# Kernel tuning notes

Hardware: AMD Instinct MI355X
Metric: run time of the kernel (lower is better)

## Reference

```python
import jax, jax.numpy as jnp
import numpy as np

# ---- MERU-style Lorentz geometry helpers (space components, implicit time) ----

def _time(x, curv):
    # x: [..., D] space component; time = sqrt(1/curv + ||x||^2)
    return jnp.sqrt(1.0 / curv + jnp.sum(x * x, axis=-1))


def pairwise_dist(x, y, curv, eps=1e-8):
    # Lorentzian inner product for all pairs: <x,y>_L = x.y - x_t*y_t  -> [N, M]
    xt = _time(x, curv)
    yt = _time(y, curv)
    inner = jnp.einsum('nd,md->nm', x, y) - xt[:, None] * yt[None, :]
    c_xyl = -curv * inner  # >= 1 on the hyperboloid
    return jnp.arccosh(jnp.clip(c_xyl, 1.0 + eps, None)) / jnp.sqrt(curv)


def oxy_angle(x, y, curv, eps=1e-8):
    # exterior angle at x of geodesic triangle (origin, x, y); elementwise over batch
    xt = _time(x, curv)
    yt = _time(y, curv)
    c_xyl = curv * (jnp.sum(x * y, axis=-1) - xt * yt)  # <= -1
    acos_numer = yt + c_xyl * xt
    acos_denom = jnp.linalg.norm(x, axis=-1) * jnp.sqrt(jnp.clip(c_xyl * c_xyl - 1.0, 0.0, None))
    acos_input = acos_numer / (acos_denom + eps)
    return jnp.arccos(jnp.clip(acos_input, -1.0 + eps, 1.0 - eps))


def half_aperture(x, curv, min_radius=0.1, eps=1e-6):
    asin_input = 2.0 * min_radius / (jnp.linalg.norm(x, axis=-1) * jnp.sqrt(curv) + eps)
    return jnp.arcsin(jnp.clip(asin_input, -1.0 + eps, 1.0 - eps))


def soft_cross_entropy(logits, target_probs):
    # torch.nn.CrossEntropyLoss with probability targets (rows need not sum to 1)
    return jnp.mean(-jnp.sum(target_probs * jax.nn.log_softmax(logits, axis=-1), axis=-1))


def entailment_loss(fa, fb, curv, eps=1e-6):
    ang = oxy_angle(fa, fb, curv)
    ap = half_aperture(fa, curv, eps=eps)
    return jnp.mean(jnp.clip(ang - ap, 0.0, None))


def setup_inputs() -> dict:
    key = jax.random.key(0)
    k1, k2, k3, k4 = jax.random.split(key, 4)
    B, D = 4096, 512
    return {
        'image_features': jax.random.normal(k1, (B, D), dtype=jnp.float32),
        'dna_features': jax.random.normal(k2, (B, D), dtype=jnp.float32),
        'text_features': jax.random.normal(k3, (B, D), dtype=jnp.float32),
        'labels': jax.random.randint(k4, (B,), 0, 500, dtype=jnp.int64),
        'logit_scale': jnp.float32(10.0),
        'curv': jnp.float32(1.0),
    }


ENTAIL_WEIGHT = 0.2


def reference(image_features, dna_features, text_features, labels, logit_scale, curv):
    # world_size == 1: gathered features == local features
    label_mat = (labels[None, :] == labels[:, None]).astype(jnp.float32)  # [B, B]

    feats = [image_features, dna_features, text_features]  # idx 0=image, 1=dna, 2=text

    contrastive_losses = []
    entail_losses = []
    for ia in range(3):
        for ib in range(3):
            if ia == ib:
                continue
            sim_ab = -pairwise_dist(feats[ia], feats[ib], curv)
            sim_ba = -pairwise_dist(feats[ib], feats[ia], curv)
            contrastive_losses.append(soft_cross_entropy(logit_scale * sim_ab, label_mat))
            contrastive_losses.append(soft_cross_entropy(logit_scale * sim_ba, label_mat))
            # 2D features branch: entailment only for (dna, image) ordering
            if ia == 1 and ib == 0:
                entail_losses.append(entailment_loss(feats[1], feats[0], curv, eps=1e-6))
            elif ia == 0 and ib == 1:
                entail_losses.append(entailment_loss(feats[1], feats[0], curv, eps=1e-6))

    contrastive_total = sum(contrastive_losses) / len(contrastive_losses)
    entail_total = sum(entail_losses) / len(entail_losses)
    total = contrastive_total + ENTAIL_WEIGHT * entail_total
    return total, contrastive_total, entail_total
```

## Files before the change

### kernel.cpp

```cpp
#include <hip/hip_runtime.h>
#include <stdint.h>

#define B_SZ 4096
#define D_SZ 512
#define SHIFT 64.0f

typedef __attribute__((ext_vector_type(4))) float floatx4;
typedef __attribute__((ext_vector_type(2))) long lng2;
typedef unsigned char u8;
typedef unsigned int u32;

#define GLD_LDS16(gp, sp)                                                              \
    __builtin_amdgcn_global_load_lds(                                                  \
        (const __attribute__((address_space(1))) void*)(gp),                           \
        (__attribute__((address_space(3))) void*)(sp), 16, 0, 0)

#define FP8MFMA(accv, av, bv)                                                          \
    accv = __builtin_amdgcn_mfma_f32_16x16x32_fp8_fp8(av, bv, accv, 0, 0, 0)

__global__ __launch_bounds__(256) void prep_kernel(
    const float* __restrict__ img, const float* __restrict__ dna,
    const float* __restrict__ txt, const float* __restrict__ curv_p,
    const int* __restrict__ labels, int* __restrict__ hist,
    u8* __restrict__ f8, float* __restrict__ times,
    float* __restrict__ zero_f, float* __restrict__ ent_partial) {
    __shared__ int lhist[512];
    __shared__ float red[4];
    int t = threadIdx.x;
    int gid = blockIdx.x * 256 + t;
    if (gid < 49155) zero_f[gid] = 0.0f;

    if (blockIdx.x == 0) {
        lhist[t] = 0; lhist[t + 256] = 0;
        __syncthreads();
        for (int n = t; n < B_SZ; n += 256) atomicAdd(&lhist[labels[n]], 1);
        __syncthreads();
        hist[t] = lhist[t]; hist[t + 256] = lhist[t + 256];
    }

    int wave = gid >> 6;
    int lane = t & 63;
    const float* src = (wave < B_SZ) ? img : (wave < 2 * B_SZ) ? dna : txt;
    int row = wave & (B_SZ - 1);
    const float* p = src + row * D_SZ + lane * 8;
    float4 v0 = *(const float4*)(p);
    float4 v1 = *(const float4*)(p + 4);
    float ss = v0.x*v0.x + v0.y*v0.y + v0.z*v0.z + v0.w*v0.w
             + v1.x*v1.x + v1.y*v1.y + v1.z*v1.z + v1.w*v1.w;
    u32 w0 = __builtin_amdgcn_cvt_pk_fp8_f32(v0.x, v0.y, 0, false);
    w0 = __builtin_amdgcn_cvt_pk_fp8_f32(v0.z, v0.w, w0, true);
    u32 w1 = __builtin_amdgcn_cvt_pk_fp8_f32(v1.x, v1.y, 0, false);
    w1 = __builtin_amdgcn_cvt_pk_fp8_f32(v1.z, v1.w, w1, true);
    uint2 pk; pk.x = w0; pk.y = w1;
    int gperm = (lane & 56) | ((lane & 3) << 1) | ((lane >> 2) & 1);
    *(uint2*)(f8 + (size_t)wave * D_SZ + gperm * 8) = pk;

    bool isdna = (wave >= B_SZ) && (wave < 2 * B_SZ);
    float dot = 0.0f, ssy = 0.0f;
    if (isdna) {
        const float* y = img + row * D_SZ + lane * 8;
        float4 y0 = *(const float4*)y, y1 = *(const float4*)(y + 4);
        dot = v0.x*y0.x + v0.y*y0.y + v0.z*y0.z + v0.w*y0.w
            + v1.x*y1.x + v1.y*y1.y + v1.z*y1.z + v1.w*y1.w;
        ssy = y0.x*y0.x + y0.y*y0.y + y0.z*y0.z + y0.w*y0.w
            + y1.x*y1.x + y1.y*y1.y + y1.z*y1.z + y1.w*y1.w;
    }
    #pragma unroll
    for (int m = 1; m < 64; m <<= 1) {
        ss += __shfl_xor(ss, m);
        if (isdna) { dot += __shfl_xor(dot, m); ssy += __shfl_xor(ssy, m); }
    }
    float curv = curv_p[0];
    float ep = 0.0f;
    if (lane == 0) {
        float xt = sqrtf(1.0f / curv + ss);
        times[wave] = xt;
        if (isdna) {
            float yt = sqrtf(1.0f / curv + ssy);
            float nx = sqrtf(ss);
            float c = curv * (dot - xt * yt);
            float numer = yt + c * xt;
            float denom = nx * sqrtf(fmaxf(c * c - 1.0f, 0.0f));
            float ai = numer / (denom + 1e-8f);
            ai = fminf(fmaxf(ai, -1.0f + 1e-8f), 1.0f - 1e-8f);
            float ang = acosf(ai);
            float as_in = 0.2f / (nx * sqrtf(curv) + 1e-6f);
            as_in = fminf(fmaxf(as_in, -1.0f + 1e-6f), 1.0f - 1e-6f);
            float ap = asinf(as_in);
            ep = fmaxf(ang - ap, 0.0f);
        }
    }
    if (blockIdx.x >= 1024 && blockIdx.x < 2048) {
        if (lane == 0) red[t >> 6] = ep;
        __syncthreads();
        if (t == 0) ent_partial[blockIdx.x - 1024] = red[0] + red[1] + red[2] + red[3];
    }
}

__global__ __launch_bounds__(512, 4) void gemm_epi_kernel(
    const u8* __restrict__ f8, const float* __restrict__ times,
    const int* __restrict__ labels,
    const float* __restrict__ ls_p, const float* __restrict__ curv_p,
    float* __restrict__ rsum_e, float* __restrict__ rsum_t,
    float* __restrict__ csum_e, float* __restrict__ csum_t) {
    __shared__ u8 sA[4][128 * 64];
    __shared__ u8 sB[4][128 * 64];

    int z = blockIdx.z;
    int pa = (z == 2) ? 1 : 0;
    int pb = (z == 0) ? 1 : 2;
    const u8* A  = f8 + (size_t)pa * (B_SZ * D_SZ);
    const u8* Bm = f8 + (size_t)pb * (B_SZ * D_SZ);

    int t = threadIdx.x;
    int rowBlk = blockIdx.y * 128;
    int colBlk = blockIdx.x * 128;
    int wave = t >> 6, lane = t & 63;
    int wr = wave >> 1;
    int wc = wave & 1;

    int chunk = (t & 3) ^ ((t >> 3) & 3);
    const u8* gA = A  + (size_t)(rowBlk + (t >> 2)) * D_SZ + chunk * 16;
    const u8* gB = Bm + (size_t)(colBlk + (t >> 2)) * D_SZ + chunk * 16;

    int q = lane >> 4, s = lane & 15;
    int slot16 = (q ^ ((s >> 1) & 3)) << 4;
    int aBase = (wr * 32 + s) * 64 + slot16;
    int bBase = (wc * 64 + s) * 64 + slot16;

    floatx4 acc[2][4];
    #pragma unroll
    for (int ii = 0; ii < 2; ++ii)
        #pragma unroll
        for (int j = 0; j < 4; ++j) acc[ii][j] = (floatx4){0.f, 0.f, 0.f, 0.f};

    {
        GLD_LDS16(gA,       &sA[0][wave * 1024]);
        GLD_LDS16(gB,       &sB[0][wave * 1024]);
        GLD_LDS16(gA + 64,  &sA[1][wave * 1024]);
        GLD_LDS16(gB + 64,  &sB[1][wave * 1024]);
        GLD_LDS16(gA + 128, &sA[2][wave * 1024]);
        GLD_LDS16(gB + 128, &sB[2][wave * 1024]);
    }

    #pragma unroll
    for (int si = 0; si < D_SZ / 64; ++si) {
        const int cur = si & 3;
        asm volatile("s_waitcnt lgkmcnt(0)" ::: "memory");
        if (si < 6)      { asm volatile("s_waitcnt vmcnt(4)" ::: "memory"); }
        else if (si == 6){ asm volatile("s_waitcnt vmcnt(2)" ::: "memory"); }
        else             { asm volatile("s_waitcnt vmcnt(0)" ::: "memory"); }
        asm volatile("s_barrier" ::: "memory");
        if (si < 5) {
            const int nxb = (si + 3) & 3;
            const int ko  = (si + 3) * 64;
            GLD_LDS16(gA + ko, &sA[nxb][wave * 1024]);
            GLD_LDS16(gB + ko, &sB[nxb][wave * 1024]);
        }
        const u8* pA = &sA[cur][0];
        const u8* pB = &sB[cur][0];
        lng2 a0 = *(const lng2*)(pA + aBase);
        lng2 a1 = *(const lng2*)(pA + aBase + 1024);
        lng2 b0 = *(const lng2*)(pB + bBase);
        lng2 b1 = *(const lng2*)(pB + bBase + 1024);
        lng2 b2 = *(const lng2*)(pB + bBase + 2048);
        lng2 b3 = *(const lng2*)(pB + bBase + 3072);
        __builtin_amdgcn_s_setprio(1);
        FP8MFMA(acc[0][0], a0.x, b0.x); FP8MFMA(acc[0][1], a0.x, b1.x);
        FP8MFMA(acc[0][2], a0.x, b2.x); FP8MFMA(acc[0][3], a0.x, b3.x);
        FP8MFMA(acc[1][0], a1.x, b0.x); FP8MFMA(acc[1][1], a1.x, b1.x);
        FP8MFMA(acc[1][2], a1.x, b2.x); FP8MFMA(acc[1][3], a1.x, b3.x);
        FP8MFMA(acc[0][0], a0.y, b0.y); FP8MFMA(acc[0][1], a0.y, b1.y);
        FP8MFMA(acc[0][2], a0.y, b2.y); FP8MFMA(acc[0][3], a0.y, b3.y);
        FP8MFMA(acc[1][0], a1.y, b0.y); FP8MFMA(acc[1][1], a1.y, b1.y);
        FP8MFMA(acc[1][2], a1.y, b2.y); FP8MFMA(acc[1][3], a1.y, b3.y);
        __builtin_amdgcn_s_setprio(0);
    }

    float ls = ls_p[0];
    float curv = curv_p[0];
    float rsc = rsqrtf(curv);
    float c2 = -ls * rsc;
    float c1 = c2 * 0.69314718f;
    float sh2p = SHIFT * 1.44269504f + c2;
    const float* tA = times + pa * B_SZ;
    const float* tB = times + pb * B_SZ;

    int rowbase = rowBlk + wr * 32;
    int colbase = colBlk + wc * 64;

    float tb[4]; int lb[4]; int mcol[4];
    #pragma unroll
    for (int j = 0; j < 4; ++j) {
        mcol[j] = colbase + j * 16 + s;
        tb[j] = tB[mcol[j]];
        lb[j] = labels[mcol[j]];
    }
    float colE[4] = {0.f, 0.f, 0.f, 0.f}, colT[4] = {0.f, 0.f, 0.f, 0.f};

    float* rsE = rsum_e + z * B_SZ;
    float* rsT = rsum_t + z * B_SZ;
    float* csE = csum_e + z * B_SZ;
    float* csT = csum_t + z * B_SZ;

    #pragma unroll
    for (int ii = 0; ii < 2; ++ii) {
        int nb = rowbase + ii * 16 + q * 4;
        float cta[4]; int la[4];
        #pragma unroll
        for (int r = 0; r < 4; ++r) { cta[r] = curv * tA[nb + r]; la[r] = labels[nb + r]; }
        float re[4] = {0.f, 0.f, 0.f, 0.f}, rt[4] = {0.f, 0.f, 0.f, 0.f};
        #pragma unroll
        for (int j = 0; j < 4; ++j) {
            floatx4 a = acc[ii][j];
            #pragma unroll
            for (int r = 0; r < 4; ++r) {
                float zc = fmaf(-curv, a[r], cta[r] * tb[j]);
                zc = fmaxf(zc, 1.0f + 1e-8f);
                float lz = __log2f(zc);
                float e = __builtin_amdgcn_exp2f(fmaf(c2, lz, sh2p));
                float tl = (la[r] == lb[j]) ? fmaf(c1, lz, c1) : 0.0f;
                re[r] += e; rt[r] += tl;
                colE[j] += e; colT[j] += tl;
            }
        }
        #pragma unroll
        for (int r = 0; r < 4; ++r) {
            #pragma unroll
            for (int m = 1; m <= 8; m <<= 1) {
                re[r] += __shfl_xor(re[r], m);
                rt[r] += __shfl_xor(rt[r], m);
            }
        }
        #pragma unroll
        for (int r = 0; r < 4; ++r) {
            if (s == r) {
                atomicAdd(&rsE[nb + r], re[r]);
                atomicAdd(&rsT[nb + r], rt[r]);
            }
        }
    }
    #pragma unroll
    for (int j = 0; j < 4; ++j) {
        colE[j] += __shfl_xor(colE[j], 16); colE[j] += __shfl_xor(colE[j], 32);
        colT[j] += __shfl_xor(colT[j], 16); colT[j] += __shfl_xor(colT[j], 32);
        if (q == 0) {
            atomicAdd(&csE[mcol[j]], colE[j]);
            atomicAdd(&csT[mcol[j]], colT[j]);
        }
    }
}

__global__ __launch_bounds__(256) void finalize_kernel(
    const float* __restrict__ rsum_e, const float* __restrict__ rsum_t,
    const float* __restrict__ csum_e, const float* __restrict__ csum_t,
    const int* __restrict__ labels, const int* __restrict__ hist,
    const float* __restrict__ ent_partial,
    float* __restrict__ ce_acc, float* __restrict__ ent_acc,
    int* __restrict__ done, float* __restrict__ out) {
    __shared__ float red[4], red2[4];
    int b = blockIdx.x, tid = threadIdx.x;
    int n = b * 256 + tid;
    float Sn = (float)hist[labels[n]];
    float part = 0.0f;
    #pragma unroll
    for (int p = 0; p < 3; ++p) {
        part += Sn * (__logf(rsum_e[p * B_SZ + n]) - SHIFT) - rsum_t[p * B_SZ + n];
        part += Sn * (__logf(csum_e[p * B_SZ + n]) - SHIFT) - csum_t[p * B_SZ + n];
    }
    float ep = (b < 4) ? ent_partial[b * 256 + tid] : 0.0f;
    #pragma unroll
    for (int m = 1; m < 64; m <<= 1) {
        part += __shfl_xor(part, m);
        ep   += __shfl_xor(ep, m);
    }
    if ((tid & 63) == 0) { red[tid >> 6] = part; red2[tid >> 6] = ep; }
    __syncthreads();
    if (tid == 0) {
        atomicAdd(ce_acc, red[0] + red[1] + red[2] + red[3]);
        atomicAdd(ent_acc, red2[0] + red2[1] + red2[2] + red2[3]);
        __threadfence();
        if (atomicAdd(done, 1) == 15) {
            float ce = atomicAdd(ce_acc, 0.0f);
            float ent = atomicAdd(ent_acc, 0.0f);
            float contr = ce / (6.0f * (float)B_SZ);
            ent /= (float)B_SZ;
            out[0] = contr + 0.2f * ent;
            out[1] = contr;
            out[2] = ent;
        }
    }
}

extern "C" void kernel_launch(void* const* d_in, const int* in_sizes, int n_in,
                              void* d_out, int out_size, void* d_ws, size_t ws_size,
                              hipStream_t stream) {
    const float* img    = (const float*)d_in[0];
    const float* dna    = (const float*)d_in[1];
    const float* txt    = (const float*)d_in[2];
    const int*   labels = (const int*)d_in[3];
    const float* ls     = (const float*)d_in[4];
    const float* curv   = (const float*)d_in[5];

    char* ws = (char*)d_ws;
    u8*    f8     = (u8*)ws;
    float* times  = (float*)(ws + 6291456);
    float* rsum_e = (float*)(ws + 6340608);
    float* rsum_t = (float*)(ws + 6389760);
    float* csum_e = (float*)(ws + 6438912);
    float* csum_t = (float*)(ws + 6488064);
    float* ce_acc = (float*)(ws + 6537216);
    float* ent_acc= (float*)(ws + 6537220);
    int*   done   = (int*)  (ws + 6537224);
    float* ent_p  = (float*)(ws + 6537228);
    int*   hist   = (int*)  (ws + 6541324);

    prep_kernel<<<3072, 256, 0, stream>>>(img, dna, txt, curv, labels, hist,
                                          f8, times, rsum_e, ent_p);
    dim3 g(32, 32, 3);
    gemm_epi_kernel<<<g, 512, 0, stream>>>(f8, times, labels, ls, curv,
                                           rsum_e, rsum_t, csum_e, csum_t);
    finalize_kernel<<<16, 256, 0, stream>>>(rsum_e, rsum_t, csum_e, csum_t,
                                            labels, hist, ent_p,
                                            ce_acc, ent_acc, done, (float*)d_out);
}
```

Before: 166.8 us.

## Make GEMM kernel persistent over six tiles with cross-tile prefetch and register double-buffering

The GEMM-epilogue kernel becomes persistent. 512 blocks each walk six consecutive 128x128 tiles instead of launching one block per tile over a 3072-block grid. The first k-slices of the next tile are prefetched into shared memory during the last k-steps of the current tile, and LDS fragments are double-buffered in registers so reads for step k+1 overlap the MFMAs of step k. The goal is to hide the pipeline fill and drain and the per-block launch overhead behind useful work. In exchange, the grid is fixed at 512 blocks, the kernel uses more registers, and the tail balance across CUs may change.

```diff
diff --git a/kernel.cpp b/kernel.cpp
--- a/kernel.cpp
+++ b/kernel.cpp
@@ -106,76 +106,15 @@
     __shared__ u8 sA[4][128 * 64];
     __shared__ u8 sB[4][128 * 64];
 
-    int z = blockIdx.z;
-    int pa = (z == 2) ? 1 : 0;
-    int pb = (z == 0) ? 1 : 2;
-    const u8* A  = f8 + (size_t)pa * (B_SZ * D_SZ);
-    const u8* Bm = f8 + (size_t)pb * (B_SZ * D_SZ);
-
     int t = threadIdx.x;
-    int rowBlk = blockIdx.y * 128;
-    int colBlk = blockIdx.x * 128;
     int wave = t >> 6, lane = t & 63;
     int wr = wave >> 1;
     int wc = wave & 1;
-
     int chunk = (t & 3) ^ ((t >> 3) & 3);
-    const u8* gA = A  + (size_t)(rowBlk + (t >> 2)) * D_SZ + chunk * 16;
-    const u8* gB = Bm + (size_t)(colBlk + (t >> 2)) * D_SZ + chunk * 16;
-
     int q = lane >> 4, s = lane & 15;
     int slot16 = (q ^ ((s >> 1) & 3)) << 4;
     int aBase = (wr * 32 + s) * 64 + slot16;
     int bBase = (wc * 64 + s) * 64 + slot16;
-
-    floatx4 acc[2][4];
-    #pragma unroll
-    for (int ii = 0; ii < 2; ++ii)
-        #pragma unroll
-        for (int j = 0; j < 4; ++j) acc[ii][j] = (floatx4){0.f, 0.f, 0.f, 0.f};
-
-    {
-        GLD_LDS16(gA,       &sA[0][wave * 1024]);
-        GLD_LDS16(gB,       &sB[0][wave * 1024]);
-        GLD_LDS16(gA + 64,  &sA[1][wave * 1024]);
-        GLD_LDS16(gB + 64,  &sB[1][wave * 1024]);
-        GLD_LDS16(gA + 128, &sA[2][wave * 1024]);
-        GLD_LDS16(gB + 128, &sB[2][wave * 1024]);
-    }
-
-    #pragma unroll
-    for (int si = 0; si < D_SZ / 64; ++si) {
-        const int cur = si & 3;
-        asm volatile("s_waitcnt lgkmcnt(0)" ::: "memory");
-        if (si < 6)      { asm volatile("s_waitcnt vmcnt(4)" ::: "memory"); }
-        else if (si == 6){ asm volatile("s_waitcnt vmcnt(2)" ::: "memory"); }
-        else             { asm volatile("s_waitcnt vmcnt(0)" ::: "memory"); }
-        asm volatile("s_barrier" ::: "memory");
-        if (si < 5) {
-            const int nxb = (si + 3) & 3;
-            const int ko  = (si + 3) * 64;
-            GLD_LDS16(gA + ko, &sA[nxb][wave * 1024]);
-            GLD_LDS16(gB + ko, &sB[nxb][wave * 1024]);
-        }
-        const u8* pA = &sA[cur][0];
-        const u8* pB = &sB[cur][0];
-        lng2 a0 = *(const lng2*)(pA + aBase);
-        lng2 a1 = *(const lng2*)(pA + aBase + 1024);
-        lng2 b0 = *(const lng2*)(pB + bBase);
-        lng2 b1 = *(const lng2*)(pB + bBase + 1024);
-        lng2 b2 = *(const lng2*)(pB + bBase + 2048);
-        lng2 b3 = *(const lng2*)(pB + bBase + 3072);
-        __builtin_amdgcn_s_setprio(1);
-        FP8MFMA(acc[0][0], a0.x, b0.x); FP8MFMA(acc[0][1], a0.x, b1.x);
-        FP8MFMA(acc[0][2], a0.x, b2.x); FP8MFMA(acc[0][3], a0.x, b3.x);
-        FP8MFMA(acc[1][0], a1.x, b0.x); FP8MFMA(acc[1][1], a1.x, b1.x);
-        FP8MFMA(acc[1][2], a1.x, b2.x); FP8MFMA(acc[1][3], a1.x, b3.x);
-        FP8MFMA(acc[0][0], a0.y, b0.y); FP8MFMA(acc[0][1], a0.y, b1.y);
-        FP8MFMA(acc[0][2], a0.y, b2.y); FP8MFMA(acc[0][3], a0.y, b3.y);
-        FP8MFMA(acc[1][0], a1.y, b0.y); FP8MFMA(acc[1][1], a1.y, b1.y);
-        FP8MFMA(acc[1][2], a1.y, b2.y); FP8MFMA(acc[1][3], a1.y, b3.y);
-        __builtin_amdgcn_s_setprio(0);
-    }
 
     float ls = ls_p[0];
     float curv = curv_p[0];
@@ -183,72 +122,174 @@
     float c2 = -ls * rsc;
     float c1 = c2 * 0.69314718f;
     float sh2p = SHIFT * 1.44269504f + c2;
-    const float* tA = times + pa * B_SZ;
-    const float* tB = times + pb * B_SZ;
-
-    int rowbase = rowBlk + wr * 32;
-    int colbase = colBlk + wc * 64;
-
-    float tb[4]; int lb[4]; int mcol[4];
-    #pragma unroll
-    for (int j = 0; j < 4; ++j) {
-        mcol[j] = colbase + j * 16 + s;
-        tb[j] = tB[mcol[j]];
-        lb[j] = labels[mcol[j]];
-    }
-    float colE[4] = {0.f, 0.f, 0.f, 0.f}, colT[4] = {0.f, 0.f, 0.f, 0.f};
-
-    float* rsE = rsum_e + z * B_SZ;
-    float* rsT = rsum_t + z * B_SZ;
-    float* csE = csum_e + z * B_SZ;
-    float* csT = csum_t + z * B_SZ;
-
-    #pragma unroll
-    for (int ii = 0; ii < 2; ++ii) {
-        int nb = rowbase + ii * 16 + q * 4;
-        float cta[4]; int la[4];
+
+    lng2 eA0, eA1, eB0, eB1, eB2, eB3;
+    lng2 oA0, oA1, oB0, oB1, oB2, oB3;
+
+#define TILE_PTRS(TL, GAV, GBV)                                                        \
+    {                                                                                  \
+        int z_ = (TL) >> 10;                                                           \
+        int rem_ = (TL) & 1023;                                                        \
+        int pa_ = (z_ == 2) ? 1 : 0;                                                   \
+        int pb_ = (z_ == 0) ? 1 : 2;                                                   \
+        GAV = f8 + (size_t)pa_ * (B_SZ * D_SZ)                                         \
+            + (size_t)(((rem_ >> 5) * 128) + (t >> 2)) * D_SZ + chunk * 16;            \
+        GBV = f8 + (size_t)pb_ * (B_SZ * D_SZ)                                         \
+            + (size_t)(((rem_ & 31) * 128) + (t >> 2)) * D_SZ + chunk * 16;            \
+    }
+
+#define KSTEP(SI, CUR, NXT, ISSUE_COND, PTRA, PTRB, VW2, DO_READ)                      \
+    do {                                                                               \
+        asm volatile("s_waitcnt lgkmcnt(0)" ::: "memory");                             \
+        if (VW2) { asm volatile("s_waitcnt vmcnt(2)" ::: "memory"); }                  \
+        else     { asm volatile("s_waitcnt vmcnt(0)" ::: "memory"); }                  \
+        asm volatile("s_barrier" ::: "memory");                                        \
+        if (ISSUE_COND) {                                                              \
+            GLD_LDS16((PTRA), &sA[(SI + 3) & 3][wave * 1024]);                         \
+            GLD_LDS16((PTRB), &sB[(SI + 3) & 3][wave * 1024]);                         \
+        }                                                                              \
+        if (DO_READ) {                                                                 \
+            const u8* pA_ = &sA[(SI + 1) & 3][0];                                      \
+            const u8* pB_ = &sB[(SI + 1) & 3][0];                                      \
+            NXT##A0 = *(const lng2*)(pA_ + aBase);                                     \
+            NXT##A1 = *(const lng2*)(pA_ + aBase + 1024);                              \
+            NXT##B0 = *(const lng2*)(pB_ + bBase);                                     \
+            NXT##B1 = *(const lng2*)(pB_ + bBase + 1024);                              \
+            NXT##B2 = *(const lng2*)(pB_ + bBase + 2048);                              \
+            NXT##B3 = *(const lng2*)(pB_ + bBase + 3072);                              \
+        }                                                                              \
+        FP8MFMA(acc[0][0], CUR##A0.x, CUR##B0.x);                                      \
+        FP8MFMA(acc[0][1], CUR##A0.x, CUR##B1.x);                                      \
+        FP8MFMA(acc[0][2], CUR##A0.x, CUR##B2.x);                                      \
+        FP8MFMA(acc[0][3], CUR##A0.x, CUR##B3.x);                                      \
+        FP8MFMA(acc[1][0], CUR##A1.x, CUR##B0.x);                                      \
+        FP8MFMA(acc[1][1], CUR##A1.x, CUR##B1.x);                                      \
+        FP8MFMA(acc[1][2], CUR##A1.x, CUR##B2.x);                                      \
+        FP8MFMA(acc[1][3], CUR##A1.x, CUR##B3.x);                                      \
+        FP8MFMA(acc[0][0], CUR##A0.y, CUR##B0.y);                                      \
+        FP8MFMA(acc[0][1], CUR##A0.y, CUR##B1.y);                                      \
+        FP8MFMA(acc[0][2], CUR##A0.y, CUR##B2.y);                                      \
+        FP8MFMA(acc[0][3], CUR##A0.y, CUR##B3.y);                                      \
+        FP8MFMA(acc[1][0], CUR##A1.y, CUR##B0.y);                                      \
+        FP8MFMA(acc[1][1], CUR##A1.y, CUR##B1.y);                                      \
+        FP8MFMA(acc[1][2], CUR##A1.y, CUR##B2.y);                                      \
+        FP8MFMA(acc[1][3], CUR##A1.y, CUR##B3.y);                                      \
+    } while (0)
+
+    const u8* gA;  const u8* gB;
+    TILE_PTRS(blockIdx.x * 6, gA, gB);
+    GLD_LDS16(gA,       &sA[0][wave * 1024]);
+    GLD_LDS16(gB,       &sB[0][wave * 1024]);
+    GLD_LDS16(gA + 64,  &sA[1][wave * 1024]);
+    GLD_LDS16(gB + 64,  &sB[1][wave * 1024]);
+    GLD_LDS16(gA + 128, &sA[2][wave * 1024]);
+    GLD_LDS16(gB + 128, &sB[2][wave * 1024]);
+    asm volatile("s_waitcnt vmcnt(4)" ::: "memory");
+    asm volatile("s_barrier" ::: "memory");
+    eA0 = *(const lng2*)(&sA[0][0] + aBase);
+    eA1 = *(const lng2*)(&sA[0][0] + aBase + 1024);
+    eB0 = *(const lng2*)(&sB[0][0] + bBase);
+    eB1 = *(const lng2*)(&sB[0][0] + bBase + 1024);
+    eB2 = *(const lng2*)(&sB[0][0] + bBase + 2048);
+    eB3 = *(const lng2*)(&sB[0][0] + bBase + 3072);
+
+    #pragma unroll 1
+    for (int tile = 0; tile < 6; ++tile) {
+        int tl = blockIdx.x * 6 + tile;
+        int z   = tl >> 10;
+        int rem = tl & 1023;
+        int rowBlk = (rem >> 5) * 128;
+        int colBlk = (rem & 31) * 128;
+        int pa = (z == 2) ? 1 : 0;
+        int pb = (z == 0) ? 1 : 2;
+        TILE_PTRS(tl, gA, gB);
+        const u8* gAx;  const u8* gBx;
+        TILE_PTRS((tl + 1 < 3072) ? (tl + 1) : 0, gAx, gBx);
+        bool nt = (tile < 5);
+
+        floatx4 acc[2][4];
         #pragma unroll
-        for (int r = 0; r < 4; ++r) { cta[r] = curv * tA[nb + r]; la[r] = labels[nb + r]; }
-        float re[4] = {0.f, 0.f, 0.f, 0.f}, rt[4] = {0.f, 0.f, 0.f, 0.f};
+        for (int ii = 0; ii < 2; ++ii)
+            #pragma unroll
+            for (int j = 0; j < 4; ++j) acc[ii][j] = (floatx4){0.f, 0.f, 0.f, 0.f};
+
+        KSTEP(0, e, o, true, gA + 3 * 64, gB + 3 * 64, true, true);
+        KSTEP(1, o, e, true, gA + 4 * 64, gB + 4 * 64, true, true);
+        KSTEP(2, e, o, true, gA + 5 * 64, gB + 5 * 64, true, true);
+        KSTEP(3, o, e, true, gA + 6 * 64, gB + 6 * 64, true, true);
+        KSTEP(4, e, o, true, gA + 7 * 64, gB + 7 * 64, true, true);
+        KSTEP(5, o, e, nt,   gAx,         gBx,         true, true);
+        KSTEP(6, e, o, nt,   gAx + 64,    gBx + 64,    nt,   true);
+        KSTEP(7, o, e, nt,   gAx + 128,   gBx + 128,   nt,   nt);
+
+        const float* tA = times + pa * B_SZ;
+        const float* tB = times + pb * B_SZ;
+        int rowbase = rowBlk + wr * 32;
+        int colbase = colBlk + wc * 64;
+
+        float tb[4]; int lb[4]; int mcol[4];
         #pragma unroll
         for (int j = 0; j < 4; ++j) {
-            floatx4 a = acc[ii][j];
+            mcol[j] = colbase + j * 16 + s;
+            tb[j] = tB[mcol[j]];
+            lb[j] = labels[mcol[j]];
+        }
+        float colE[4] = {0.f, 0.f, 0.f, 0.f}, colT[4] = {0.f, 0.f, 0.f, 0.f};
+
+        float* rsE = rsum_e + z * B_SZ;
+        float* rsT = rsum_t + z * B_SZ;
+        float* csE = csum_e + z * B_SZ;
+        float* csT = csum_t + z * B_SZ;
+
+        #pragma unroll
+        for (int ii = 0; ii < 2; ++ii) {
+            int nb = rowbase + ii * 16 + q * 4;
+            float cta[4]; int la[4];
+            #pragma unroll
+            for (int r = 0; r < 4; ++r) { cta[r] = curv * tA[nb + r]; la[r] = labels[nb + r]; }
+            float re[4] = {0.f, 0.f, 0.f, 0.f}, rt[4] = {0.f, 0.f, 0.f, 0.f};
+            #pragma unroll
+            for (int j = 0; j < 4; ++j) {
+                floatx4 a = acc[ii][j];
+                #pragma unroll
+                for (int r = 0; r < 4; ++r) {
+                    float zc = fmaf(-curv, a[r], cta[r] * tb[j]);
+                    zc = fmaxf(zc, 1.0f + 1e-8f);
+                    float lz = __log2f(zc);
+                    float e = __builtin_amdgcn_exp2f(fmaf(c2, lz, sh2p));
+                    float tl2 = (la[r] == lb[j]) ? fmaf(c1, lz, c1) : 0.0f;
+                    re[r] += e; rt[r] += tl2;
+                    colE[j] += e; colT[j] += tl2;
+                }
+            }
             #pragma unroll
             for (int r = 0; r < 4; ++r) {
-                float zc = fmaf(-curv, a[r], cta[r] * tb[j]);
-                zc = fmaxf(zc, 1.0f + 1e-8f);
-                float lz = __log2f(zc);
-                float e = __builtin_amdgcn_exp2f(fmaf(c2, lz, sh2p));
-                float tl = (la[r] == lb[j]) ? fmaf(c1, lz, c1) : 0.0f;
-                re[r] += e; rt[r] += tl;
-                colE[j] += e; colT[j] += tl;
+                #pragma unroll
+                for (int m = 1; m <= 8; m <<= 1) {
+                    re[r] += __shfl_xor(re[r], m);
+                    rt[r] += __shfl_xor(rt[r], m);
+                }
             }
+            #pragma unroll
+            for (int r = 0; r < 4; ++r) {
+                if (s == r) {
+                    atomicAdd(&rsE[nb + r], re[r]);
+                    atomicAdd(&rsT[nb + r], rt[r]);
+                }
+            }
         }
         #pragma unroll
-        for (int r = 0; r < 4; ++r) {
-            #pragma unroll
-            for (int m = 1; m <= 8; m <<= 1) {
-                re[r] += __shfl_xor(re[r], m);
-                rt[r] += __shfl_xor(rt[r], m);
+        for (int j = 0; j < 4; ++j) {
+            colE[j] += __shfl_xor(colE[j], 16); colE[j] += __shfl_xor(colE[j], 32);
+            colT[j] += __shfl_xor(colT[j], 16); colT[j] += __shfl_xor(colT[j], 32);
+            if (q == 0) {
+                atomicAdd(&csE[mcol[j]], colE[j]);
+                atomicAdd(&csT[mcol[j]], colT[j]);
             }
         }
-        #pragma unroll
-        for (int r = 0; r < 4; ++r) {
-            if (s == r) {
-                atomicAdd(&rsE[nb + r], re[r]);
-                atomicAdd(&rsT[nb + r], rt[r]);
-            }
-        }
-    }
-    #pragma unroll
-    for (int j = 0; j < 4; ++j) {
-        colE[j] += __shfl_xor(colE[j], 16); colE[j] += __shfl_xor(colE[j], 32);
-        colT[j] += __shfl_xor(colT[j], 16); colT[j] += __shfl_xor(colT[j], 32);
-        if (q == 0) {
-            atomicAdd(&csE[mcol[j]], colE[j]);
-            atomicAdd(&csT[mcol[j]], colT[j]);
-        }
-    }
+    }
+#undef KSTEP
+#undef TILE_PTRS
 }
 
 __global__ __launch_bounds__(256) void finalize_kernel(
@@ -317,9 +358,8 @@
 
     prep_kernel<<<3072, 256, 0, stream>>>(img, dna, txt, curv, labels, hist,
                                           f8, times, rsum_e, ent_p);
-    dim3 g(32, 32, 3);
-    gemm_epi_kernel<<<g, 512, 0, stream>>>(f8, times, labels, ls, curv,
-                                           rsum_e, rsum_t, csum_e, csum_t);
+    gemm_epi_kernel<<<512, 512, 0, stream>>>(f8, times, labels, ls, curv,
+                                             rsum_e, rsum_t, csum_e, csum_t);
     finalize_kernel<<<16, 256, 0, stream>>>(rsum_e, rsum_t, csum_e, csum_t,
                                             labels, hist, ent_p,
                                             ce_acc, ent_acc, done, (float*)d_out);
```

After: 150.4 us, median of 2. 1.11x faster.
